# Performance work log

Measured on AMD Instinct MI355X. Metric: run time of the kernel, lower is better.

The kernel has to match this reference:

```python
import jax, jax.numpy as jnp
import numpy as np
from jax import lax

B, T, I, H, L, C = 128, 784, 1, 256, 20, 10  # batch, seq_len, input, hidden, layers, classes


def setup_inputs() -> dict:
    key = jax.random.key(0)
    ks = jax.random.split(key, 9)
    s = 1.0 / np.sqrt(H)  # torch nn.RNN init: U(-1/sqrt(H), 1/sqrt(H))
    u = lambda k, shape: jax.random.uniform(k, shape, jnp.float32, -s, s)
    return {
        "x": jax.random.normal(ks[0], (B, T, I), jnp.float32),
        "W_ih0": u(ks[1], (H, I)),        # layer 0 input proj
        "b_ih0": u(ks[2], (H,)),
        "W_ih": u(ks[3], (L - 1, H, H)),  # layers 1..L-1 input proj
        "b_ih": u(ks[4], (L - 1, H)),
        "W_hh": u(ks[5], (L, H, H)),      # recurrent weights, all layers
        "b_hh": u(ks[6], (L, H)),
        "W_fc": u(ks[7], (C, H)),         # classification head
        "b_fc": u(ks[8], (C,)),
    }


def _rnn_layer(x_seq, W_ih, b_ih, W_hh, b_hh):
    """One vanilla relu-RNN layer. x_seq: [B,T,in] -> [B,T,H]."""
    # Hoist the input projection out of the scan (batched GEMM over all timesteps).
    xp = jnp.einsum('bti,hi->bth', x_seq, W_ih) + b_ih  # [B,T,H]
    h0 = jnp.zeros((x_seq.shape[0], W_hh.shape[0]), x_seq.dtype)

    def step(h, xt):
        h = jax.nn.relu(xt + h @ W_hh.T + b_hh)
        return h, h

    _, ys = lax.scan(step, h0, jnp.swapaxes(xp, 0, 1))  # scan over time
    return jnp.swapaxes(ys, 0, 1)  # [B,T,H]


def reference(x, W_ih0, b_ih0, W_ih, b_ih, W_hh, b_hh, W_fc, b_fc):
    h = _rnn_layer(x, W_ih0, b_ih0, W_hh[0], b_hh[0])
    for l in range(L - 1):  # fixed small layer loop
        h = _rnn_layer(h, W_ih[l], b_ih[l], W_hh[l + 1], b_hh[l + 1])
    last_hidden = h[:, -1, :]  # [B,H]
    return last_hidden @ W_fc.T + b_fc  # [B,C]
```

## Files before the change

kernel.cpp:

```cpp
#include <hip/hip_runtime.h>
#include <hip/hip_fp16.h>


#define B_    128
#define T_    784
#define H_    256
#define L_    20
#define C_    10
#define G_    8
#define BM_   16
#define S_    4
#define NS_   196
#define SW_   280
#define RQWS_ 4096
#define TPB_  512

typedef _Float16 v8h __attribute__((ext_vector_type(8)));
typedef _Float16 v4h __attribute__((ext_vector_type(4)));
typedef float    v4f __attribute__((ext_vector_type(4)));
typedef unsigned long long u64;

union U64H { u64 u; _Float16 h[4]; };

__global__ __launch_bounds__(TPB_, 2)
void rnn_wavefront(const float* __restrict__ x,
                   const float* __restrict__ W_ih0,
                   const float* __restrict__ b_ih0,
                   const float* __restrict__ W_ih,
                   const float* __restrict__ b_ih,
                   const float* __restrict__ W_hh,
                   const float* __restrict__ b_hh,
                   const float* __restrict__ W_fc,
                   const float* __restrict__ b_fc,
                   float* __restrict__ out,
                   unsigned* __restrict__ prod,
                   unsigned* __restrict__ cons,
                   u64* __restrict__ ring,
                   int rmask)
{
    const int l    = blockIdx.x >> 3;
    const int g    = blockIdx.x & 7;
    const int tid  = threadIdx.x;
    const int lane = tid & 63;
    const int wave = tid >> 6;
    const int quad = lane >> 4;
    const int s16  = lane & 15;
    const int nbase = wave * 32;
    const int m_e  = tid >> 5;
    const int n_e  = (tid & 31) * 8;

    __shared__ __align__(16) _Float16 bufX[S_][BM_][SW_];
    __shared__ __align__(16) _Float16 lH[2][BM_][SW_];

    for (int i = tid; i < 2 * BM_ * SW_; i += TPB_) (&lH[0][0][0])[i] = (_Float16)0.f;

    v8h wf[16][2];
#pragma unroll
    for (int kt = 0; kt < 16; ++kt) {
        const int k0 = kt * 32 + quad * 8;
#pragma unroll
        for (int nt = 0; nt < 2; ++nt) {
            const int j = nbase + nt * 16 + s16;
            v8h w;
            if (kt < 8) {
                if (l == 0) {
#pragma unroll
                    for (int i = 0; i < 8; ++i) w[i] = (_Float16)0.f;
                } else {
                    const float* src = &W_ih[(((size_t)(l - 1) * H_) + j) * H_ + k0];
#pragma unroll
                    for (int i = 0; i < 8; ++i) w[i] = (_Float16)src[i];
                }
            } else {
                const float* src = &W_hh[(((size_t)l * H_) + j) * H_ + (k0 - 256)];
#pragma unroll
                for (int i = 0; i < 8; ++i) w[i] = (_Float16)src[i];
            }
            wf[kt][nt] = w;
        }
    }

    float bias[2][4], w0v[2][4];
#pragma unroll
    for (int nt = 0; nt < 2; ++nt)
#pragma unroll
        for (int r = 0; r < 4; ++r) {
            const int j = nbase + nt * 16 + quad * 4 + r;
            bias[nt][r] = b_hh[l * H_ + j] + ((l == 0) ? b_ih0[j] : b_ih[(l - 1) * H_ + j]);
            w0v[nt][r]  = (l == 0) ? W_ih0[j] : 0.f;
        }

    unsigned* upprod = prod + ((l > 0 ? l - 1 : 0) * G_ + g);
    unsigned* myprod = prod + (l * G_ + g);
    unsigned* mycons = cons + (l * G_ + g);
    unsigned* dncons = cons + (((l < L_ - 1) ? l + 1 : l) * G_ + g);
    const unsigned R = (unsigned)rmask + 1u;
    u64* myring = ring + ((size_t)(l * G_ + g) * (size_t)R) * RQWS_;
    u64* upring = ring + ((size_t)((l > 0 ? l - 1 : 0) * G_ + g) * (size_t)R) * RQWS_;

    unsigned pSeen = 0, cSeen = 0;
    const size_t eidx = (size_t)m_e * 64 + (size_t)(tid & 31) * 2;

    if (l > 0) {
        if (tid == 64) {
            while (pSeen < 2u) {
                pSeen = __hip_atomic_load(upprod, __ATOMIC_RELAXED,
                                          __HIP_MEMORY_SCOPE_AGENT);
                if (pSeen < 2u) __builtin_amdgcn_s_sleep(2);
            }
        }
        __syncthreads();
#pragma unroll
        for (int jj = 0; jj < S_; ++jj) {
            u64 v0 = __hip_atomic_load(upring + (size_t)jj * 1024 + eidx,
                                       __ATOMIC_RELAXED, __HIP_MEMORY_SCOPE_AGENT);
            u64 v1 = __hip_atomic_load(upring + (size_t)jj * 1024 + eidx + 1,
                                       __ATOMIC_RELAXED, __HIP_MEMORY_SCOPE_AGENT);
            *(u64*)&bufX[jj][m_e][n_e]     = v0;
            *(u64*)&bufX[jj][m_e][n_e + 4] = v1;
        }
    }

    for (int s = 0; s < NS_; ++s) {
        const bool pfOK = (l > 0) && (s + 1 < NS_);
        u64 pfv[S_][2];
        v4h XPh[S_][2];

#pragma unroll
        for (int j = 0; j < S_; ++j) {
            const int t = S_ * s + j;
            __syncthreads();

            if (j == 0) {
                if (tid == 0 && l > 0)
                    __hip_atomic_store(mycons, (unsigned)(s + 1), __ATOMIC_RELAXED,
                                       __HIP_MEMORY_SCOPE_AGENT);
                if (tid == 64 && pfOK) {
                    const unsigned tgt = (unsigned)(s + 2);
                    while (pSeen < tgt) {
                        pSeen = __hip_atomic_load(upprod, __ATOMIC_RELAXED,
                                                  __HIP_MEMORY_SCOPE_AGENT);
                        if (pSeen < tgt) __builtin_amdgcn_s_sleep(2);
                    }
                }
                if (tid == 128 && l < L_ - 1 && s >= (int)R) {
                    const unsigned tgt = (unsigned)(s - (int)R + 1);
                    while (cSeen < tgt) {
                        cSeen = __hip_atomic_load(dncons, __ATOMIC_RELAXED,
                                                  __HIP_MEMORY_SCOPE_AGENT);
                        if (cSeen < tgt) __builtin_amdgcn_s_sleep(2);
                    }
                }

                if (l > 0) {
                    v4f xpa[S_][2];
#pragma unroll
                    for (int jj = 0; jj < S_; ++jj)
#pragma unroll
                        for (int nt = 0; nt < 2; ++nt)
                            xpa[jj][nt] = (v4f){bias[nt][0], bias[nt][1],
                                                bias[nt][2], bias[nt][3]};
#pragma unroll
                    for (int jj = 0; jj < S_; ++jj) {
#pragma unroll
                        for (int kt = 0; kt < 8; ++kt) {
                            v8h a = *(const v8h*)&bufX[jj][s16][kt * 32 + quad * 8];
                            xpa[jj][0] = __builtin_amdgcn_mfma_f32_16x16x32_f16(wf[kt][0], a, xpa[jj][0], 0, 0, 0);
                            xpa[jj][1] = __builtin_amdgcn_mfma_f32_16x16x32_f16(wf[kt][1], a, xpa[jj][1], 0, 0, 0);
                        }
                    }
#pragma unroll
                    for (int jj = 0; jj < S_; ++jj)
#pragma unroll
                        for (int nt = 0; nt < 2; ++nt)
#pragma unroll
                            for (int r = 0; r < 4; ++r)
                                XPh[jj][nt][r] = (_Float16)xpa[jj][nt][r];
                } else {
#pragma unroll
                    for (int jj = 0; jj < S_; ++jj) {
                        const float xv = x[(size_t)(g * BM_ + s16) * T_ + (S_ * s + jj)];
#pragma unroll
                        for (int nt = 0; nt < 2; ++nt)
#pragma unroll
                            for (int r = 0; r < 4; ++r)
                                XPh[jj][nt][r] = (_Float16)(bias[nt][r] + xv * w0v[nt][r]);
                    }
                }
            }

            if (j == 1) {
                if (tid == 0 && l < L_ - 1 && s >= 1)
                    __hip_atomic_store(myprod, (unsigned)s, __ATOMIC_RELAXED,
                                       __HIP_MEMORY_SCOPE_AGENT);
                if (pfOK) {
                    const u64* base = upring + (size_t)((s + 1) & rmask) * RQWS_;
#pragma unroll
                    for (int jj = 0; jj < S_; ++jj) {
                        pfv[jj][0] = __hip_atomic_load(base + (size_t)jj * 1024 + eidx,
                                                       __ATOMIC_RELAXED,
                                                       __HIP_MEMORY_SCOPE_AGENT);
                        pfv[jj][1] = __hip_atomic_load(base + (size_t)jj * 1024 + eidx + 1,
                                                       __ATOMIC_RELAXED,
                                                       __HIP_MEMORY_SCOPE_AGENT);
                    }
                }
            }

            if (l < L_ - 1 && t > 0) {
                u64 e0 = *(const u64*)&lH[t & 1][m_e][n_e];
                u64 e1 = *(const u64*)&lH[t & 1][m_e][n_e + 4];
                u64* d = myring + (size_t)(((t - 1) >> 2) & rmask) * RQWS_
                                + (size_t)((t - 1) & 3) * 1024 + eidx;
                __hip_atomic_store(d,     e0, __ATOMIC_RELAXED, __HIP_MEMORY_SCOPE_AGENT);
                __hip_atomic_store(d + 1, e1, __ATOMIC_RELAXED, __HIP_MEMORY_SCOPE_AGENT);
            }

            v4f acc0 = (v4f){0.f, 0.f, 0.f, 0.f};
            v4f acc1 = (v4f){0.f, 0.f, 0.f, 0.f};
#pragma unroll
            for (int kt = 8; kt < 16; ++kt) {
                v8h a = *(const v8h*)&lH[t & 1][s16][(kt - 8) * 32 + quad * 8];
                acc0 = __builtin_amdgcn_mfma_f32_16x16x32_f16(wf[kt][0], a, acc0, 0, 0, 0);
                acc1 = __builtin_amdgcn_mfma_f32_16x16x32_f16(wf[kt][1], a, acc1, 0, 0, 0);
            }

#pragma unroll
            for (int nt = 0; nt < 2; ++nt) {
                const v4f av = nt ? acc1 : acc0;
                U64H pk;
#pragma unroll
                for (int r = 0; r < 4; ++r) {
                    float v = (float)XPh[j][nt][r] + av[r];
                    v = fmaxf(v, 0.f);
                    pk.h[r] = (_Float16)v;
                }
                *(u64*)&lH[(t + 1) & 1][s16][nbase + nt * 16 + quad * 4] = pk.u;
            }

            if (j == S_ - 1) {
                __syncthreads();
                if (pfOK) {
#pragma unroll
                    for (int jj = 0; jj < S_; ++jj) {
                        *(u64*)&bufX[jj][m_e][n_e]     = pfv[jj][0];
                        *(u64*)&bufX[jj][m_e][n_e + 4] = pfv[jj][1];
                    }
                }
            }
        }
    }

    if (l < L_ - 1) {
        u64 e0 = *(const u64*)&lH[0][m_e][n_e];
        u64 e1 = *(const u64*)&lH[0][m_e][n_e + 4];
        u64* d = myring + (size_t)(((T_ - 1) >> 2) & rmask) * RQWS_
                        + (size_t)3 * 1024 + eidx;
        __hip_atomic_store(d,     e0, __ATOMIC_RELAXED, __HIP_MEMORY_SCOPE_AGENT);
        __hip_atomic_store(d + 1, e1, __ATOMIC_RELAXED, __HIP_MEMORY_SCOPE_AGENT);
        __syncthreads();
        if (tid == 0)
            __hip_atomic_store(myprod, (unsigned)NS_, __ATOMIC_RELAXED,
                               __HIP_MEMORY_SCOPE_AGENT);
    } else {
        __syncthreads();
        if (tid < BM_ * C_) {
            const int bl = tid / C_;
            const int c  = tid % C_;
            float sum = b_fc[c];
            for (int k = 0; k < H_; ++k) sum += (float)lH[0][bl][k] * W_fc[c * H_ + k];
            out[(size_t)(g * BM_ + bl) * C_ + c] = sum;
        }
    }
}

extern "C" void kernel_launch(void* const* d_in, const int* in_sizes, int n_in,
                              void* d_out, int out_size, void* d_ws, size_t ws_size,
                              hipStream_t stream) {
    const float* x     = (const float*)d_in[0];
    const float* W_ih0 = (const float*)d_in[1];
    const float* b_ih0 = (const float*)d_in[2];
    const float* W_ih  = (const float*)d_in[3];
    const float* b_ih  = (const float*)d_in[4];
    const float* W_hh  = (const float*)d_in[5];
    const float* b_hh  = (const float*)d_in[6];
    const float* W_fc  = (const float*)d_in[7];
    const float* b_fc  = (const float*)d_in[8];
    float* out = (float*)d_out;

    const size_t cntBytes = (size_t)L_ * G_ * sizeof(unsigned);
    unsigned* prod = (unsigned*)d_ws;
    unsigned* cons = (unsigned*)((char*)d_ws + cntBytes);
    u64* ring      = (u64*)((char*)d_ws + 2 * cntBytes);

    const size_t slotBytes = (size_t)RQWS_ * 8;
    const size_t base = 2 * cntBytes;
    int R = 4;
    if (ws_size >= base + (size_t)L_ * G_ * 16 * slotBytes) R = 16;
    else if (ws_size >= base + (size_t)L_ * G_ * 8 * slotBytes) R = 8;

    hipMemsetAsync(d_ws, 0, 2 * cntBytes, stream);

    rnn_wavefront<<<dim3(L_ * G_), dim3(TPB_), 0, stream>>>(
        x, W_ih0, b_ih0, W_ih, b_ih, W_hh, b_hh, W_fc, b_fc,
        out, prod, cons, ring, R - 1);
}
```

Baseline: 1.105 ms.

## Halve block to four waves, each computing four N-tiles of the recurrence

Cuts threads per block from 512 to 256 (8 waves to 4). Each wave now covers 64 output columns with four MFMA accumulators instead of two, and each thread copies twice as many ring elements. The aim is cheaper __syncthreads barriers on the serial per-timestep critical path and more MFMA work per wave. The cost is higher register pressure (64 weight fragments per thread, launch bounds relaxed to 1 block per CU) and fewer waves to hide MFMA and LDS latency.

After: 1.606 ms. +45.3%, slower.

```diff
diff --git a/kernel.cpp b/kernel.cpp
--- a/kernel.cpp
+++ b/kernel.cpp
@@ -13,7 +13,8 @@
 #define NS_   196
 #define SW_   280
 #define RQWS_ 4096
-#define TPB_  512
+#define TPB_  256
+#define NT_   4
 
 typedef _Float16 v8h __attribute__((ext_vector_type(8)));
 typedef _Float16 v4h __attribute__((ext_vector_type(4)));
@@ -22,7 +23,7 @@
 
 union U64H { u64 u; _Float16 h[4]; };
 
-__global__ __launch_bounds__(TPB_, 2)
+__global__ __launch_bounds__(TPB_, 1)
 void rnn_wavefront(const float* __restrict__ x,
                    const float* __restrict__ W_ih0,
                    const float* __restrict__ b_ih0,
@@ -45,7 +46,7 @@
     const int wave = tid >> 6;
     const int quad = lane >> 4;
     const int s16  = lane & 15;
-    const int nbase = wave * 32;
+    const int nbase = wave * 64;
     const int m_e  = tid >> 5;
     const int n_e  = (tid & 31) * 8;
 
@@ -54,12 +55,12 @@
 
     for (int i = tid; i < 2 * BM_ * SW_; i += TPB_) (&lH[0][0][0])[i] = (_Float16)0.f;
 
-    v8h wf[16][2];
+    v8h wf[16][NT_];
 #pragma unroll
     for (int kt = 0; kt < 16; ++kt) {
         const int k0 = kt * 32 + quad * 8;
 #pragma unroll
-        for (int nt = 0; nt < 2; ++nt) {
+        for (int nt = 0; nt < NT_; ++nt) {
             const int j = nbase + nt * 16 + s16;
             v8h w;
             if (kt < 8) {
@@ -80,9 +81,9 @@
         }
     }
 
-    float bias[2][4], w0v[2][4];
-#pragma unroll
-    for (int nt = 0; nt < 2; ++nt)
+    float bias[NT_][4], w0v[NT_][4];
+#pragma unroll
+    for (int nt = 0; nt < NT_; ++nt)
 #pragma unroll
         for (int r = 0; r < 4; ++r) {
             const int j = nbase + nt * 16 + quad * 4 + r;
@@ -116,15 +117,21 @@
                                        __ATOMIC_RELAXED, __HIP_MEMORY_SCOPE_AGENT);
             u64 v1 = __hip_atomic_load(upring + (size_t)jj * 1024 + eidx + 1,
                                        __ATOMIC_RELAXED, __HIP_MEMORY_SCOPE_AGENT);
-            *(u64*)&bufX[jj][m_e][n_e]     = v0;
-            *(u64*)&bufX[jj][m_e][n_e + 4] = v1;
+            u64 v2 = __hip_atomic_load(upring + (size_t)jj * 1024 + eidx + 512,
+                                       __ATOMIC_RELAXED, __HIP_MEMORY_SCOPE_AGENT);
+            u64 v3 = __hip_atomic_load(upring + (size_t)jj * 1024 + eidx + 513,
+                                       __ATOMIC_RELAXED, __HIP_MEMORY_SCOPE_AGENT);
+            *(u64*)&bufX[jj][m_e][n_e]         = v0;
+            *(u64*)&bufX[jj][m_e][n_e + 4]     = v1;
+            *(u64*)&bufX[jj][m_e + 8][n_e]     = v2;
+            *(u64*)&bufX[jj][m_e + 8][n_e + 4] = v3;
         }
     }
 
     for (int s = 0; s < NS_; ++s) {
         const bool pfOK = (l > 0) && (s + 1 < NS_);
-        u64 pfv[S_][2];
-        v4h XPh[S_][2];
+        u64 pfv[S_][4];
+        v4h XPh[S_][NT_];
 
 #pragma unroll
         for (int j = 0; j < S_; ++j) {
@@ -153,35 +160,33 @@
                 }
 
                 if (l > 0) {
-                    v4f xpa[S_][2];
-#pragma unroll
-                    for (int jj = 0; jj < S_; ++jj)
-#pragma unroll
-                        for (int nt = 0; nt < 2; ++nt)
-                            xpa[jj][nt] = (v4f){bias[nt][0], bias[nt][1],
-                                                bias[nt][2], bias[nt][3]};
 #pragma unroll
                     for (int jj = 0; jj < S_; ++jj) {
+                        v4f xpa[NT_];
+#pragma unroll
+                        for (int nt = 0; nt < NT_; ++nt)
+                            xpa[nt] = (v4f){bias[nt][0], bias[nt][1],
+                                            bias[nt][2], bias[nt][3]};
 #pragma unroll
                         for (int kt = 0; kt < 8; ++kt) {
                             v8h a = *(const v8h*)&bufX[jj][s16][kt * 32 + quad * 8];
-                            xpa[jj][0] = __builtin_amdgcn_mfma_f32_16x16x32_f16(wf[kt][0], a, xpa[jj][0], 0, 0, 0);
-                            xpa[jj][1] = __builtin_amdgcn_mfma_f32_16x16x32_f16(wf[kt][1], a, xpa[jj][1], 0, 0, 0);
+#pragma unroll
+                            for (int nt = 0; nt < NT_; ++nt)
+                                xpa[nt] = __builtin_amdgcn_mfma_f32_16x16x32_f16(
+                                              wf[kt][nt], a, xpa[nt], 0, 0, 0);
                         }
-                    }
-#pragma unroll
-                    for (int jj = 0; jj < S_; ++jj)
-#pragma unroll
-                        for (int nt = 0; nt < 2; ++nt)
+#pragma unroll
+                        for (int nt = 0; nt < NT_; ++nt)
 #pragma unroll
                             for (int r = 0; r < 4; ++r)
-                                XPh[jj][nt][r] = (_Float16)xpa[jj][nt][r];
+                                XPh[jj][nt][r] = (_Float16)xpa[nt][r];
+                    }
                 } else {
 #pragma unroll
                     for (int jj = 0; jj < S_; ++jj) {
                         const float xv = x[(size_t)(g * BM_ + s16) * T_ + (S_ * s + jj)];
 #pragma unroll
-                        for (int nt = 0; nt < 2; ++nt)
+                        for (int nt = 0; nt < NT_; ++nt)
 #pragma unroll
                             for (int r = 0; r < 4; ++r)
                                 XPh[jj][nt][r] = (_Float16)(bias[nt][r] + xv * w0v[nt][r]);
@@ -203,6 +208,12 @@
                         pfv[jj][1] = __hip_atomic_load(base + (size_t)jj * 1024 + eidx + 1,
                                                        __ATOMIC_RELAXED,
                                                        __HIP_MEMORY_SCOPE_AGENT);
+                        pfv[jj][2] = __hip_atomic_load(base + (size_t)jj * 1024 + eidx + 512,
+                                                       __ATOMIC_RELAXED,
+                                                       __HIP_MEMORY_SCOPE_AGENT);
+                        pfv[jj][3] = __hip_atomic_load(base + (size_t)jj * 1024 + eidx + 513,
+                                                       __ATOMIC_RELAXED,
+                                                       __HIP_MEMORY_SCOPE_AGENT);
                     }
                 }
             }
@@ -210,28 +221,34 @@
             if (l < L_ - 1 && t > 0) {
                 u64 e0 = *(const u64*)&lH[t & 1][m_e][n_e];
                 u64 e1 = *(const u64*)&lH[t & 1][m_e][n_e + 4];
+                u64 e2 = *(const u64*)&lH[t & 1][m_e + 8][n_e];
+                u64 e3 = *(const u64*)&lH[t & 1][m_e + 8][n_e + 4];
                 u64* d = myring + (size_t)(((t - 1) >> 2) & rmask) * RQWS_
                                 + (size_t)((t - 1) & 3) * 1024 + eidx;
-                __hip_atomic_store(d,     e0, __ATOMIC_RELAXED, __HIP_MEMORY_SCOPE_AGENT);
-                __hip_atomic_store(d + 1, e1, __ATOMIC_RELAXED, __HIP_MEMORY_SCOPE_AGENT);
-            }
-
-            v4f acc0 = (v4f){0.f, 0.f, 0.f, 0.f};
-            v4f acc1 = (v4f){0.f, 0.f, 0.f, 0.f};
-#pragma unroll
-            for (int kt = 8; kt < 16; ++kt) {
-                v8h a = *(const v8h*)&lH[t & 1][s16][(kt - 8) * 32 + quad * 8];
-                acc0 = __builtin_amdgcn_mfma_f32_16x16x32_f16(wf[kt][0], a, acc0, 0, 0, 0);
-                acc1 = __builtin_amdgcn_mfma_f32_16x16x32_f16(wf[kt][1], a, acc1, 0, 0, 0);
-            }
-
-#pragma unroll
-            for (int nt = 0; nt < 2; ++nt) {
-                const v4f av = nt ? acc1 : acc0;
+                __hip_atomic_store(d,       e0, __ATOMIC_RELAXED, __HIP_MEMORY_SCOPE_AGENT);
+                __hip_atomic_store(d + 1,   e1, __ATOMIC_RELAXED, __HIP_MEMORY_SCOPE_AGENT);
+                __hip_atomic_store(d + 512, e2, __ATOMIC_RELAXED, __HIP_MEMORY_SCOPE_AGENT);
+                __hip_atomic_store(d + 513, e3, __ATOMIC_RELAXED, __HIP_MEMORY_SCOPE_AGENT);
+            }
+
+            v4f acc[NT_];
+#pragma unroll
+            for (int nt = 0; nt < NT_; ++nt) acc[nt] = (v4f){0.f, 0.f, 0.f, 0.f};
+#pragma unroll
+            for (int kt = 0; kt < 8; ++kt) {
+                v8h a = *(const v8h*)&lH[t & 1][s16][kt * 32 + quad * 8];
+#pragma unroll
+                for (int nt = 0; nt < NT_; ++nt)
+                    acc[nt] = __builtin_amdgcn_mfma_f32_16x16x32_f16(
+                                  wf[8 + kt][nt], a, acc[nt], 0, 0, 0);
+            }
+
+#pragma unroll
+            for (int nt = 0; nt < NT_; ++nt) {
                 U64H pk;
 #pragma unroll
                 for (int r = 0; r < 4; ++r) {
-                    float v = (float)XPh[j][nt][r] + av[r];
+                    float v = (float)XPh[j][nt][r] + acc[nt][r];
                     v = fmaxf(v, 0.f);
                     pk.h[r] = (_Float16)v;
                 }
@@ -243,8 +260,10 @@
                 if (pfOK) {
 #pragma unroll
                     for (int jj = 0; jj < S_; ++jj) {
-                        *(u64*)&bufX[jj][m_e][n_e]     = pfv[jj][0];
-                        *(u64*)&bufX[jj][m_e][n_e + 4] = pfv[jj][1];
+                        *(u64*)&bufX[jj][m_e][n_e]         = pfv[jj][0];
+                        *(u64*)&bufX[jj][m_e][n_e + 4]     = pfv[jj][1];
+                        *(u64*)&bufX[jj][m_e + 8][n_e]     = pfv[jj][2];
+                        *(u64*)&bufX[jj][m_e + 8][n_e + 4] = pfv[jj][3];
                     }
                 }
             }
@@ -254,10 +273,14 @@
     if (l < L_ - 1) {
         u64 e0 = *(const u64*)&lH[0][m_e][n_e];
         u64 e1 = *(const u64*)&lH[0][m_e][n_e + 4];
+        u64 e2 = *(const u64*)&lH[0][m_e + 8][n_e];
+        u64 e3 = *(const u64*)&lH[0][m_e + 8][n_e + 4];
         u64* d = myring + (size_t)(((T_ - 1) >> 2) & rmask) * RQWS_
                         + (size_t)3 * 1024 + eidx;
-        __hip_atomic_store(d,     e0, __ATOMIC_RELAXED, __HIP_MEMORY_SCOPE_AGENT);
-        __hip_atomic_store(d + 1, e1, __ATOMIC_RELAXED, __HIP_MEMORY_SCOPE_AGENT);
+        __hip_atomic_store(d,       e0, __ATOMIC_RELAXED, __HIP_MEMORY_SCOPE_AGENT);
+        __hip_atomic_store(d + 1,   e1, __ATOMIC_RELAXED, __HIP_MEMORY_SCOPE_AGENT);
+        __hip_atomic_store(d + 512, e2, __ATOMIC_RELAXED, __HIP_MEMORY_SCOPE_AGENT);
+        __hip_atomic_store(d + 513, e3, __ATOMIC_RELAXED, __HIP_MEMORY_SCOPE_AGENT);
         __syncthreads();
         if (tid == 0)
             __hip_atomic_store(myprod, (unsigned)NS_, __ATOMIC_RELAXED,
```
